# Optimization experiments

Measured on AMD Instinct MI355X. Metric: run time of the kernel, lower is better.

## Reference

```python
import jax, jax.numpy as jnp
import numpy as np

B, K, D = 8, 4000, 256
H, DQ, DV = 8, 32, 32
WIN, PAD = 200, 50
STEP = WIN - 2 * PAD  # 100
BETA = 0.25


def setup_inputs() -> dict:
    key = jax.random.key(0)
    ks = jax.random.split(key, 14)
    s = 0.02
    return {
        "query": jax.random.normal(ks[0], (B, K, D), jnp.float32),
        "key": jax.random.normal(ks[1], (B, K, D), jnp.float32),
        "value": jax.random.normal(ks[2], (B, K, D), jnp.float32),
        "Wq": jax.random.normal(ks[3], (D, H * DQ), jnp.float32) * s,
        "bq": jax.random.normal(ks[4], (H * DQ,), jnp.float32) * s,
        "Wk": jax.random.normal(ks[5], (D, H * DQ), jnp.float32) * s,
        "bk": jax.random.normal(ks[6], (H * DQ,), jnp.float32) * s,
        "Wv": jax.random.normal(ks[7], (D, H * DV), jnp.float32) * s,
        "bv": jax.random.normal(ks[8], (H * DV,), jnp.float32) * s,
        "Wo": jax.random.normal(ks[9], (H * DV, D), jnp.float32) * s,
        "bo": jax.random.normal(ks[10], (D,), jnp.float32) * s,
    }


def _windows(x, n_win):
    starts = jnp.arange(n_win) * STEP
    idx = starts[:, None] + jnp.arange(WIN)[None, :]
    return x[:, :, idx, :]


def reference(query, key, value, Wq, bq, Wk, bk, Wv, bv, Wo, bo):
    b, k_len, d = query.shape
    pad = lambda t: jnp.pad(t, ((0, 0), (PAD, PAD), (0, 0)), mode='edge')  # replicate pad
    qp, kp, vp = pad(query), pad(key), pad(value)
    kpad = k_len + 2 * PAD
    n_win = (kpad - WIN) // STEP + 1

    def proj(x, Wm, bias, dh):
        y = x @ Wm + bias                       # [B, Kp, H*dh]
        return y.reshape(b, kpad, H, dh).transpose(0, 2, 1, 3)  # [B, H, Kp, dh]

    q = _windows(proj(qp, Wq, bq, DQ), n_win)
    kk = _windows(proj(kp, Wk, bk, DQ), n_win)
    v = _windows(proj(vp, Wv, bv, DV), n_win)

    scores = jnp.einsum('bhnid,bhnjd->bhnij', q, kk) / jnp.sqrt(jnp.float32(WIN))
    dist = jnp.abs(jnp.arange(WIN)[:, None] - jnp.arange(WIN)[None, :]).astype(scores.dtype)
    cauchy = (1.0 / (1.0 + BETA * dist * dist)) * (1.0 - jnp.eye(WIN, dtype=scores.dtype))
    scores = scores * cauchy
    causal = jnp.triu(jnp.ones((WIN, WIN), dtype=bool), k=1)  # attention_size is not None -> causal masking
    scores = jnp.where(causal, -jnp.inf, scores)
    attn = jax.nn.softmax(scores, axis=-1)
    out = jnp.einsum('bhnij,bhnjd->bhnid', attn, v)
    out = out[:, :, :, PAD:WIN - PAD, :].reshape(b, H, k_len, DV)
    out = out.transpose(0, 2, 1, 3).reshape(b, k_len, H * DV)  # heads concatenated, head-major slices
    return out @ Wo + bo
```

## Files before the change

kernel.cpp:

```cpp
#include <hip/hip_runtime.h>


typedef __bf16 bf16_t;
typedef __bf16 bf16x8 __attribute__((ext_vector_type(8)));
typedef float  f32x4  __attribute__((ext_vector_type(4)));

#define MFMA16(a, b, c) __builtin_amdgcn_mfma_f32_16x16x32_bf16((a), (b), (c), 0, 0, 0)

static __device__ __forceinline__ bf16x8 cvt8(float4 a, float4 b) {
  bf16x8 r;
  r[0] = (bf16_t)a.x; r[1] = (bf16_t)a.y; r[2] = (bf16_t)a.z; r[3] = (bf16_t)a.w;
  r[4] = (bf16_t)b.x; r[5] = (bf16_t)b.y; r[6] = (bf16_t)b.z; r[7] = (bf16_t)b.w;
  return r;
}

static __device__ __forceinline__ unsigned short bbits(bf16_t v) {
  union { bf16_t b; unsigned short u; } c; c.b = v; return c.u;
}

__global__ __launch_bounds__(256)
void prep_weights(const float* __restrict__ Wq, const float* __restrict__ Wk,
                  const float* __restrict__ Wv, const float* __restrict__ Wo,
                  bf16_t* __restrict__ wt) {
  const int mat  = blockIdx.x >> 6;
  const int tile = blockIdx.x & 63;
  const int kt = (tile >> 3) * 32, nt = (tile & 7) * 32;
  const float* W = (mat == 0) ? Wq : (mat == 1) ? Wk : (mat == 2) ? Wv : Wo;
  __shared__ float t[32][33];
  const int tx = threadIdx.x & 31, ty = threadIdx.x >> 5;
#pragma unroll
  for (int i = 0; i < 32; i += 8)
    t[ty + i][tx] = W[(size_t)(kt + ty + i) * 256 + nt + tx];
  __syncthreads();
  bf16_t* dst = wt + (size_t)mat * 65536;
#pragma unroll
  for (int i = 0; i < 32; i += 8)
    dst[(size_t)(nt + ty + i) * 256 + kt + tx] = (bf16_t)t[tx][ty + i];
}

__global__ __launch_bounds__(256)
void proj_gemm(const float* __restrict__ qx, const float* __restrict__ kx,
               const float* __restrict__ vx, const bf16_t* __restrict__ wt,
               const float* __restrict__ bq, const float* __restrict__ bk,
               const float* __restrict__ bv,
               bf16_t* __restrict__ qb, bf16_t* __restrict__ kb,
               bf16_t* __restrict__ vt, int M, float qscale) {
  const int mode = blockIdx.y;
  const float* X    = (mode == 0) ? qx : (mode == 1) ? kx : vx;
  const float* bias = (mode == 0) ? bq : (mode == 1) ? bk : bv;
  const bf16_t* W   = wt + (size_t)mode * 65536;

  __shared__ bf16_t la[64 * 40];
  __shared__ bf16_t lb[256 * 40];
  const int tid  = threadIdx.x;
  const int lane = tid & 63;
  const int wv   = tid >> 6;
  const int lo   = lane & 15, hi = lane >> 4;
  const int m0   = blockIdx.x * 64;
  int ar = m0 + (tid >> 2); if (ar >= M) ar = M - 1;
  const int acg  = (tid & 3) * 8;
  const int brow = tid >> 2;
  const int bcg  = (tid & 3) * 8;

  f32x4 acc[4][4] = {};

  for (int kk = 0; kk < 256; kk += 32) {
    {
      const float* ap = X + (size_t)ar * 256 + kk + acg;
      *(bf16x8*)&la[(tid >> 2) * 40 + acg] =
          cvt8(((const float4*)ap)[0], ((const float4*)ap)[1]);
    }
#pragma unroll
    for (int rr = 0; rr < 4; ++rr) {
      const int row = brow + rr * 64;
      *(bf16x8*)&lb[row * 40 + bcg] =
          *(const bf16x8*)&W[(size_t)row * 256 + kk + bcg];
    }
    __syncthreads();

    bf16x8 af[4], bfv[4];
#pragma unroll
    for (int mi = 0; mi < 4; ++mi)
      af[mi] = *(const bf16x8*)&la[(mi * 16 + lo) * 40 + hi * 8];
#pragma unroll
    for (int ni = 0; ni < 4; ++ni)
      bfv[ni] = *(const bf16x8*)&lb[(wv * 64 + ni * 16 + lo) * 40 + hi * 8];
#pragma unroll
    for (int mi = 0; mi < 4; ++mi)
#pragma unroll
      for (int ni = 0; ni < 4; ++ni)
        acc[mi][ni] = MFMA16(af[mi], bfv[ni], acc[mi][ni]);
    __syncthreads();
  }

#pragma unroll
  for (int mi = 0; mi < 4; ++mi) {
    const int mb = m0 + mi * 16 + hi * 4;
    if (mb >= M) continue;
#pragma unroll
    for (int ni = 0; ni < 4; ++ni) {
      const int n = wv * 64 + ni * 16 + lo;
      const float bia = bias[n];
      if (mode == 0) {
#pragma unroll
        for (int r = 0; r < 4; ++r)
          qb[(size_t)(mb + r) * 256 + n] = (bf16_t)((acc[mi][ni][r] + bia) * qscale);
      } else if (mode == 1) {
        const int b = mb / 4000, t = mb - b * 4000;
#pragma unroll
        for (int r = 0; r < 4; ++r)
          kb[((size_t)b * 4064 + t + 50 + r) * 256 + n] = (bf16_t)(acc[mi][ni][r] + bia);
      } else {
        const int b = mb / 4000, t = mb - b * 4000;
        const int h = n >> 5, dv = n & 31;
        bf16_t* O = vt + ((size_t)((b * 8 + h) * 32 + dv)) * 4064 + t + 50;
        unsigned short e0 = bbits((bf16_t)(acc[mi][ni][0] + bia));
        unsigned short e1 = bbits((bf16_t)(acc[mi][ni][1] + bia));
        unsigned short e2 = bbits((bf16_t)(acc[mi][ni][2] + bia));
        unsigned short e3 = bbits((bf16_t)(acc[mi][ni][3] + bia));
        unsigned* O32 = (unsigned*)O;
        O32[0] = (unsigned)e0 | ((unsigned)e1 << 16);
        O32[1] = (unsigned)e2 | ((unsigned)e3 << 16);
      }
    }
  }
}

__global__ __launch_bounds__(256)
void out_gemm(const bf16_t* __restrict__ ao, const bf16_t* __restrict__ wt,
              const float* __restrict__ bias, float* __restrict__ Out, int M) {
  __shared__ bf16_t la[64 * 40];
  __shared__ bf16_t lb[256 * 40];
  const int tid  = threadIdx.x;
  const int lane = tid & 63;
  const int wv   = tid >> 6;
  const int lo   = lane & 15, hi = lane >> 4;
  const int m0   = blockIdx.x * 64;
  int ar = m0 + (tid >> 2); if (ar >= M) ar = M - 1;
  const int acg  = (tid & 3) * 8;
  const int brow = tid >> 2;
  const int bcg  = (tid & 3) * 8;

  f32x4 acc[4][4] = {};

  for (int kk = 0; kk < 256; kk += 32) {
    *(bf16x8*)&la[(tid >> 2) * 40 + acg] =
        *(const bf16x8*)&ao[(size_t)ar * 256 + kk + acg];
#pragma unroll
    for (int rr = 0; rr < 4; ++rr) {
      const int row = brow + rr * 64;
      *(bf16x8*)&lb[row * 40 + bcg] =
          *(const bf16x8*)&wt[(size_t)row * 256 + kk + bcg];
    }
    __syncthreads();

    bf16x8 af[4], bfv[4];
#pragma unroll
    for (int mi = 0; mi < 4; ++mi)
      af[mi] = *(const bf16x8*)&la[(mi * 16 + lo) * 40 + hi * 8];
#pragma unroll
    for (int ni = 0; ni < 4; ++ni)
      bfv[ni] = *(const bf16x8*)&lb[(wv * 64 + ni * 16 + lo) * 40 + hi * 8];
#pragma unroll
    for (int mi = 0; mi < 4; ++mi)
#pragma unroll
      for (int ni = 0; ni < 4; ++ni)
        acc[mi][ni] = MFMA16(af[mi], bfv[ni], acc[mi][ni]);
    __syncthreads();
  }

#pragma unroll
  for (int mi = 0; mi < 4; ++mi) {
    const int mb = m0 + mi * 16 + hi * 4;
    if (mb >= M) continue;
#pragma unroll
    for (int ni = 0; ni < 4; ++ni) {
      const int n = wv * 64 + ni * 16 + lo;
      const float bia = bias[n];
#pragma unroll
      for (int r = 0; r < 4; ++r)
        Out[(size_t)(mb + r) * 256 + n] = acc[mi][ni][r] + bia;
    }
  }
}

__global__ void fill_edges(bf16_t* __restrict__ kb, bf16_t* __restrict__ vt, int nb) {
  const int idx = blockIdx.x * 256 + threadIdx.x;
  const int kcnt = nb * 64 * 256;
  if (idx < kcnt) {
    const int b  = idx >> 14;
    const int pp = (idx >> 8) & 63;
    const int nn = idx & 255;
    const int p  = (pp < 50) ? pp : pp + 4000;
    bf16_t v = (pp < 50) ? kb[((size_t)b * 4064 + 50) * 256 + nn] : (bf16_t)0.f;
    kb[((size_t)b * 4064 + p) * 256 + nn] = v;
  } else {
    const int j  = idx - kcnt;
    const int bh = j >> 11;
    const int dv = (j >> 6) & 31;
    const int pp = j & 63;
    const int p  = (pp < 50) ? pp : pp + 4000;
    bf16_t v = (pp < 50) ? vt[((size_t)bh * 32 + dv) * 4064 + 50] : (bf16_t)0.f;
    vt[((size_t)bh * 32 + dv) * 4064 + p] = v;
  }
}

__global__ __launch_bounds__(448)
void attn_win(const bf16_t* __restrict__ qb, const bf16_t* __restrict__ kb,
              const bf16_t* __restrict__ vt, bf16_t* __restrict__ ao) {
  const int blk = blockIdx.x;
  const int n = blk % 40;
  const int h = (blk / 40) & 7;
  const int b = blk / 320;
  const int wv = threadIdx.x >> 6;
  const int lane = threadIdx.x & 63;
  const int lo = lane & 15, hi = lane >> 4;

  __shared__ __align__(16) bf16_t E[7][16][40];

  const int i0 = 50 + 16 * wv;
  int jtmax = (65 + 16 * wv) >> 4;
  if (jtmax > 9) jtmax = 9;
  const int reach = jtmax * 16 + 16;

  int tq = n * 100 + 16 * wv + lo;
  if (tq > 3999) tq = 3999;
  const bf16x8 qf = *(const bf16x8*)&qb[((size_t)b * 4000 + tq) * 256 + h * 32 + hi * 8];

  const f32x4 zero = {0.f, 0.f, 0.f, 0.f};
  bf16x8 onesf;
#pragma unroll
  for (int u = 0; u < 8; ++u) onesf[u] = (bf16_t)1.0f;

  f32x4 o0 = zero, o1 = zero, sm = zero;
  const size_t vbase = ((size_t)((b * 8 + h) * 32)) * 4064 + n * 100;
  const size_t kbase = ((size_t)(b * 4064 + n * 100)) * 256 + h * 32 + hi * 8;
  const int dbase = i0 + hi * 4 - lo;

#pragma unroll
  for (int kt = 0; kt < 5; ++kt) if (kt * 32 < reach) {
#pragma unroll
    for (int half = 0; half < 2; ++half) {
      const int jt = kt * 2 + half;
      if (jt <= jtmax) {
        const bf16x8 kf = *(const bf16x8*)&kb[kbase + (size_t)(jt * 16 + lo) * 256];
        const f32x4 s = MFMA16(qf, kf, zero);
#pragma unroll
        for (int r = 0; r < 4; ++r) {
          const int d = dbase + r - jt * 16;
          const float df = (float)d;
          float c = __builtin_amdgcn_rcpf(__builtin_fmaf(0.25f * df, df, 1.f));
          c = (d == 0) ? 0.f : c;
          float e = __expf(s[r] * c);
          e = (d < 0) ? 0.f : e;
          E[wv][hi * 4 + r][half * 16 + lo] = (bf16_t)e;
        }
      } else {
#pragma unroll
        for (int r = 0; r < 4; ++r)
          E[wv][hi * 4 + r][half * 16 + lo] = (bf16_t)0.f;
      }
    }
    const bf16x8 pf = *(const bf16x8*)&E[wv][lo][hi * 8];
    const bf16x8 v0 = *(const bf16x8*)&vt[vbase + (size_t)lo * 4064 + kt * 32 + hi * 8];
    const bf16x8 v1 = *(const bf16x8*)&vt[vbase + (size_t)(16 + lo) * 4064 + kt * 32 + hi * 8];
    o0 = MFMA16(pf, v0, o0);
    o1 = MFMA16(pf, v1, o1);
    sm = MFMA16(pf, onesf, sm);
  }

#pragma unroll
  for (int r = 0; r < 4; ++r) {
    const int i = i0 + hi * 4 + r;
    if (i < 150) {
      const float ri = __builtin_amdgcn_rcpf(sm[r]);
      const int t = n * 100 + i - 50;
      bf16_t* op = &ao[((size_t)b * 4000 + t) * 256 + h * 32];
      op[lo]      = (bf16_t)(o0[r] * ri);
      op[16 + lo] = (bf16_t)(o1[r] * ri);
    }
  }
}

extern "C" void kernel_launch(void* const* d_in, const int* in_sizes, int n_in,
                              void* d_out, int out_size, void* d_ws, size_t ws_size,
                              hipStream_t stream) {
  (void)in_sizes; (void)n_in; (void)out_size;
  const float* query = (const float*)d_in[0];
  const float* key   = (const float*)d_in[1];
  const float* value = (const float*)d_in[2];
  const float* Wq = (const float*)d_in[3];
  const float* bq = (const float*)d_in[4];
  const float* Wk = (const float*)d_in[5];
  const float* bk = (const float*)d_in[6];
  const float* Wv = (const float*)d_in[7];
  const float* bv = (const float*)d_in[8];
  const float* Wo = (const float*)d_in[9];
  const float* bo = (const float*)d_in[10];

  int bc = 8;
  while (bc > 1 && 524288ull + (unsigned long long)bc * 8257536ull > (unsigned long long)ws_size)
    bc >>= 1;

  bf16_t* wt = (bf16_t*)d_ws;
  bf16_t* qb = wt + 4 * 65536;
  bf16_t* kb = qb + (size_t)bc * 4000 * 256;
  bf16_t* vt = kb + (size_t)bc * 4064 * 256;
  bf16_t* ao = vt + (size_t)bc * 8 * 32 * 4064;

  prep_weights<<<256, 256, 0, stream>>>(Wq, Wk, Wv, Wo, wt);

  const float qscale = 0.07071067811865475f;

  for (int b0 = 0; b0 < 8; b0 += bc) {
    const int M = bc * 4000;
    const int mblk = (M + 63) / 64;
    const float* qx = query + (size_t)b0 * 4000 * 256;
    const float* kx = key   + (size_t)b0 * 4000 * 256;
    const float* vx = value + (size_t)b0 * 4000 * 256;
    float* ox = (float*)d_out + (size_t)b0 * 4000 * 256;

    proj_gemm<<<dim3(mblk, 3), 256, 0, stream>>>(qx, kx, vx, wt, bq, bk, bv,
                                                 qb, kb, vt, M, qscale);
    fill_edges<<<bc * 128, 256, 0, stream>>>(kb, vt, bc);
    attn_win<<<bc * 320, 448, 0, stream>>>(qb, kb, vt, ao);
    out_gemm<<<dim3(mblk), 256, 0, stream>>>(ao, wt + 3 * 65536, bo, ox, M);
  }
}
```

Measured before the change: 97.24 us.

## Hold weight fragments in registers and stage full A tile once in GEMMs

```diff
diff --git a/kernel.cpp b/kernel.cpp
--- a/kernel.cpp
+++ b/kernel.cpp
@@ -38,7 +38,9 @@
     dst[(size_t)(nt + ty + i) * 256 + kt + tx] = (bf16_t)t[tx][ty + i];
 }
 
-__global__ __launch_bounds__(256)
+#define LDSA_BYTES (32 * 1040)
+
+__global__ __launch_bounds__(256, 2)
 void proj_gemm(const float* __restrict__ qx, const float* __restrict__ kx,
                const float* __restrict__ vx, const bf16_t* __restrict__ wt,
                const float* __restrict__ bq, const float* __restrict__ bk,
@@ -50,47 +52,45 @@
   const float* bias = (mode == 0) ? bq : (mode == 1) ? bk : bv;
   const bf16_t* W   = wt + (size_t)mode * 65536;
 
-  __shared__ bf16_t la[64 * 40];
-  __shared__ bf16_t lb[256 * 40];
+  __shared__ __align__(16) char lds_a[LDSA_BYTES];
   const int tid  = threadIdx.x;
   const int lane = tid & 63;
   const int wv   = tid >> 6;
   const int lo   = lane & 15, hi = lane >> 4;
   const int m0   = blockIdx.x * 64;
-  int ar = m0 + (tid >> 2); if (ar >= M) ar = M - 1;
-  const int acg  = (tid & 3) * 8;
-  const int brow = tid >> 2;
-  const int bcg  = (tid & 3) * 8;
+  const int r    = tid >> 2;
+  const int q    = tid & 3;
+  int ar = m0 + r; if (ar >= M) ar = M - 1;
+
+  bf16x8 breg[8][4];
+#pragma unroll
+  for (int kk = 0; kk < 8; ++kk)
+#pragma unroll
+    for (int ni = 0; ni < 4; ++ni)
+      breg[kk][ni] =
+          *(const bf16x8*)&W[(size_t)(wv * 64 + ni * 16 + lo) * 256 + kk * 32 + hi * 8];
+
+#pragma unroll
+  for (int i = 0; i < 8; ++i) {
+    const int c = q * 8 + i;
+    const float* ap = X + (size_t)ar * 256 + c * 8;
+    const bf16x8 v = cvt8(((const float4*)ap)[0], ((const float4*)ap)[1]);
+    *(bf16x8*)(lds_a + c * 1040 + r * 16) = v;
+  }
+  __syncthreads();
 
   f32x4 acc[4][4] = {};
-
-  for (int kk = 0; kk < 256; kk += 32) {
-    {
-      const float* ap = X + (size_t)ar * 256 + kk + acg;
-      *(bf16x8*)&la[(tid >> 2) * 40 + acg] =
-          cvt8(((const float4*)ap)[0], ((const float4*)ap)[1]);
-    }
-#pragma unroll
-    for (int rr = 0; rr < 4; ++rr) {
-      const int row = brow + rr * 64;
-      *(bf16x8*)&lb[row * 40 + bcg] =
-          *(const bf16x8*)&W[(size_t)row * 256 + kk + bcg];
-    }
-    __syncthreads();
-
-    bf16x8 af[4], bfv[4];
+#pragma unroll
+  for (int kk = 0; kk < 8; ++kk) {
+    bf16x8 af[4];
 #pragma unroll
     for (int mi = 0; mi < 4; ++mi)
-      af[mi] = *(const bf16x8*)&la[(mi * 16 + lo) * 40 + hi * 8];
-#pragma unroll
-    for (int ni = 0; ni < 4; ++ni)
-      bfv[ni] = *(const bf16x8*)&lb[(wv * 64 + ni * 16 + lo) * 40 + hi * 8];
+      af[mi] = *(const bf16x8*)(lds_a + (kk * 4 + hi) * 1040 + (mi * 16 + lo) * 16);
 #pragma unroll
     for (int mi = 0; mi < 4; ++mi)
 #pragma unroll
       for (int ni = 0; ni < 4; ++ni)
-        acc[mi][ni] = MFMA16(af[mi], bfv[ni], acc[mi][ni]);
-    __syncthreads();
+        acc[mi][ni] = MFMA16(af[mi], breg[kk][ni], acc[mi][ni]);
   }
 
 #pragma unroll
@@ -103,13 +103,13 @@
       const float bia = bias[n];
       if (mode == 0) {
 #pragma unroll
-        for (int r = 0; r < 4; ++r)
-          qb[(size_t)(mb + r) * 256 + n] = (bf16_t)((acc[mi][ni][r] + bia) * qscale);
+        for (int rr = 0; rr < 4; ++rr)
+          qb[(size_t)(mb + rr) * 256 + n] = (bf16_t)((acc[mi][ni][rr] + bia) * qscale);
       } else if (mode == 1) {
         const int b = mb / 4000, t = mb - b * 4000;
 #pragma unroll
-        for (int r = 0; r < 4; ++r)
-          kb[((size_t)b * 4064 + t + 50 + r) * 256 + n] = (bf16_t)(acc[mi][ni][r] + bia);
+        for (int rr = 0; rr < 4; ++rr)
+          kb[((size_t)b * 4064 + t + 50 + rr) * 256 + n] = (bf16_t)(acc[mi][ni][rr] + bia);
       } else {
         const int b = mb / 4000, t = mb - b * 4000;
         const int h = n >> 5, dv = n & 31;
@@ -126,47 +126,47 @@
   }
 }
 
-__global__ __launch_bounds__(256)
+__global__ __launch_bounds__(256, 2)
 void out_gemm(const bf16_t* __restrict__ ao, const bf16_t* __restrict__ wt,
               const float* __restrict__ bias, float* __restrict__ Out, int M) {
-  __shared__ bf16_t la[64 * 40];
-  __shared__ bf16_t lb[256 * 40];
+  __shared__ __align__(16) char lds_a[LDSA_BYTES];
   const int tid  = threadIdx.x;
   const int lane = tid & 63;
   const int wv   = tid >> 6;
   const int lo   = lane & 15, hi = lane >> 4;
   const int m0   = blockIdx.x * 64;
-  int ar = m0 + (tid >> 2); if (ar >= M) ar = M - 1;
-  const int acg  = (tid & 3) * 8;
-  const int brow = tid >> 2;
-  const int bcg  = (tid & 3) * 8;
+  const int r    = tid >> 2;
+  const int q    = tid & 3;
+  int ar = m0 + r; if (ar >= M) ar = M - 1;
+
+  bf16x8 breg[8][4];
+#pragma unroll
+  for (int kk = 0; kk < 8; ++kk)
+#pragma unroll
+    for (int ni = 0; ni < 4; ++ni)
+      breg[kk][ni] =
+          *(const bf16x8*)&wt[(size_t)(wv * 64 + ni * 16 + lo) * 256 + kk * 32 + hi * 8];
+
+#pragma unroll
+  for (int i = 0; i < 8; ++i) {
+    const int c = q * 8 + i;
+    const bf16x8 v = *(const bf16x8*)&ao[(size_t)ar * 256 + c * 8];
+    *(bf16x8*)(lds_a + c * 1040 + r * 16) = v;
+  }
+  __syncthreads();
 
   f32x4 acc[4][4] = {};
-
-  for (int kk = 0; kk < 256; kk += 32) {
-    *(bf16x8*)&la[(tid >> 2) * 40 + acg] =
-        *(const bf16x8*)&ao[(size_t)ar * 256 + kk + acg];
-#pragma unroll
-    for (int rr = 0; rr < 4; ++rr) {
-      const int row = brow + rr * 64;
-      *(bf16x8*)&lb[row * 40 + bcg] =
-          *(const bf16x8*)&wt[(size_t)row * 256 + kk + bcg];
-    }
-    __syncthreads();
-
-    bf16x8 af[4], bfv[4];
+#pragma unroll
+  for (int kk = 0; kk < 8; ++kk) {
+    bf16x8 af[4];
 #pragma unroll
     for (int mi = 0; mi < 4; ++mi)
-      af[mi] = *(const bf16x8*)&la[(mi * 16 + lo) * 40 + hi * 8];
-#pragma unroll
-    for (int ni = 0; ni < 4; ++ni)
-      bfv[ni] = *(const bf16x8*)&lb[(wv * 64 + ni * 16 + lo) * 40 + hi * 8];
+      af[mi] = *(const bf16x8*)(lds_a + (kk * 4 + hi) * 1040 + (mi * 16 + lo) * 16);
 #pragma unroll
     for (int mi = 0; mi < 4; ++mi)
 #pragma unroll
       for (int ni = 0; ni < 4; ++ni)
-        acc[mi][ni] = MFMA16(af[mi], bfv[ni], acc[mi][ni]);
-    __syncthreads();
+        acc[mi][ni] = MFMA16(af[mi], breg[kk][ni], acc[mi][ni]);
   }
 
 #pragma unroll
@@ -178,8 +178,8 @@
       const int n = wv * 64 + ni * 16 + lo;
       const float bia = bias[n];
 #pragma unroll
-      for (int r = 0; r < 4; ++r)
-        Out[(size_t)(mb + r) * 256 + n] = acc[mi][ni][r] + bia;
+      for (int rr = 0; rr < 4; ++rr)
+        Out[(size_t)(mb + rr) * 256 + n] = acc[mi][ni][rr] + bia;
     }
   }
 }
```

Measured after the change: 119.5 us. +22.9%, slower.

## Retile projection and output GEMMs to 128x128 with direct global-to-LDS loads

Applied to the files above, without the earlier changes.

```diff
diff --git a/kernel.cpp b/kernel.cpp
--- a/kernel.cpp
+++ b/kernel.cpp
@@ -6,6 +6,13 @@
 typedef float  f32x4  __attribute__((ext_vector_type(4)));
 
 #define MFMA16(a, b, c) __builtin_amdgcn_mfma_f32_16x16x32_bf16((a), (b), (c), 0, 0, 0)
+
+typedef __attribute__((address_space(1))) const unsigned char gas_u8;
+typedef __attribute__((address_space(3))) unsigned char las_u8;
+
+static __device__ __forceinline__ void gload16(const void* g, void* l) {
+  __builtin_amdgcn_global_load_lds((gas_u8*)g, (las_u8*)l, 16, 0, 0);
+}
 
 static __device__ __forceinline__ bf16x8 cvt8(float4 a, float4 b) {
   bf16x8 r;
@@ -38,6 +45,7 @@
     dst[(size_t)(nt + ty + i) * 256 + kt + tx] = (bf16_t)t[tx][ty + i];
 }
 
+
 __global__ __launch_bounds__(256)
 void proj_gemm(const float* __restrict__ qx, const float* __restrict__ kx,
                const float* __restrict__ vx, const bf16_t* __restrict__ wt,
@@ -45,46 +53,65 @@
                const float* __restrict__ bv,
                bf16_t* __restrict__ qb, bf16_t* __restrict__ kb,
                bf16_t* __restrict__ vt, int M, float qscale) {
-  const int mode = blockIdx.y;
+  const int mode = blockIdx.z;
   const float* X    = (mode == 0) ? qx : (mode == 1) ? kx : vx;
   const float* bias = (mode == 0) ? bq : (mode == 1) ? bk : bv;
   const bf16_t* W   = wt + (size_t)mode * 65536;
 
-  __shared__ bf16_t la[64 * 40];
-  __shared__ bf16_t lb[256 * 40];
+  __shared__ bf16_t la[128 * 40];
+  __shared__ __align__(16) char ldsB[8192];
   const int tid  = threadIdx.x;
   const int lane = tid & 63;
-  const int wv   = tid >> 6;
+  const int w4   = tid >> 6;
+  const int wr   = ((tid >> 7) & 1) * 64;
+  const int wc   = ((tid >> 6) & 1) * 64;
   const int lo   = lane & 15, hi = lane >> 4;
-  const int m0   = blockIdx.x * 64;
-  int ar = m0 + (tid >> 2); if (ar >= M) ar = M - 1;
-  const int acg  = (tid & 3) * 8;
-  const int brow = tid >> 2;
-  const int bcg  = (tid & 3) * 8;
+  const int m0   = blockIdx.x * 128;
+  const int n0   = blockIdx.y * 128;
+  const int arow = tid >> 1;
+  const int acol = (tid & 1) * 16;
+  int ar = m0 + arow; if (ar >= M) ar = M - 1;
+
+  const bf16_t* bsrc[2];
+  char* bldst[2];
+#pragma unroll
+  for (int j = 0; j < 2; ++j) {
+    const int s = (w4 * 2 + j) * 64 + lane;
+    const int row = s >> 2, cs = s & 3;
+    const int c = cs ^ ((row >> 2) & 3);
+    bsrc[j]  = W + (size_t)(n0 + row) * 256 + c * 8;
+    bldst[j] = ldsB + (w4 * 2 + j) * 1024;
+  }
+  int bbase[4];
+#pragma unroll
+  for (int ni = 0; ni < 4; ++ni) {
+    const int row = wc + ni * 16 + lo;
+    bbase[ni] = (row * 4 + (hi ^ ((lo >> 2) & 3))) * 16;
+  }
 
   f32x4 acc[4][4] = {};
 
   for (int kk = 0; kk < 256; kk += 32) {
     {
-      const float* ap = X + (size_t)ar * 256 + kk + acg;
-      *(bf16x8*)&la[(tid >> 2) * 40 + acg] =
-          cvt8(((const float4*)ap)[0], ((const float4*)ap)[1]);
-    }
-#pragma unroll
-    for (int rr = 0; rr < 4; ++rr) {
-      const int row = brow + rr * 64;
-      *(bf16x8*)&lb[row * 40 + bcg] =
-          *(const bf16x8*)&W[(size_t)row * 256 + kk + bcg];
-    }
+      const float* ap = X + (size_t)ar * 256 + kk + acol;
+      float4 x0 = ((const float4*)ap)[0];
+      float4 x1 = ((const float4*)ap)[1];
+      float4 x2 = ((const float4*)ap)[2];
+      float4 x3 = ((const float4*)ap)[3];
+      *(bf16x8*)&la[arow * 40 + acol]     = cvt8(x0, x1);
+      *(bf16x8*)&la[arow * 40 + acol + 8] = cvt8(x2, x3);
+    }
+    gload16(bsrc[0] + kk, bldst[0]);
+    gload16(bsrc[1] + kk, bldst[1]);
     __syncthreads();
 
     bf16x8 af[4], bfv[4];
 #pragma unroll
     for (int mi = 0; mi < 4; ++mi)
-      af[mi] = *(const bf16x8*)&la[(mi * 16 + lo) * 40 + hi * 8];
+      af[mi] = *(const bf16x8*)&la[(wr + mi * 16 + lo) * 40 + hi * 8];
 #pragma unroll
     for (int ni = 0; ni < 4; ++ni)
-      bfv[ni] = *(const bf16x8*)&lb[(wv * 64 + ni * 16 + lo) * 40 + hi * 8];
+      bfv[ni] = *(const bf16x8*)(ldsB + bbase[ni]);
 #pragma unroll
     for (int mi = 0; mi < 4; ++mi)
 #pragma unroll
@@ -95,21 +122,21 @@
 
 #pragma unroll
   for (int mi = 0; mi < 4; ++mi) {
-    const int mb = m0 + mi * 16 + hi * 4;
+    const int mb = m0 + wr + mi * 16 + hi * 4;
     if (mb >= M) continue;
 #pragma unroll
     for (int ni = 0; ni < 4; ++ni) {
-      const int n = wv * 64 + ni * 16 + lo;
+      const int n = n0 + wc + ni * 16 + lo;
       const float bia = bias[n];
       if (mode == 0) {
 #pragma unroll
-        for (int r = 0; r < 4; ++r)
-          qb[(size_t)(mb + r) * 256 + n] = (bf16_t)((acc[mi][ni][r] + bia) * qscale);
+        for (int rr = 0; rr < 4; ++rr)
+          qb[(size_t)(mb + rr) * 256 + n] = (bf16_t)((acc[mi][ni][rr] + bia) * qscale);
       } else if (mode == 1) {
         const int b = mb / 4000, t = mb - b * 4000;
 #pragma unroll
-        for (int r = 0; r < 4; ++r)
-          kb[((size_t)b * 4064 + t + 50 + r) * 256 + n] = (bf16_t)(acc[mi][ni][r] + bia);
+        for (int rr = 0; rr < 4; ++rr)
+          kb[((size_t)b * 4064 + t + 50 + rr) * 256 + n] = (bf16_t)(acc[mi][ni][rr] + bia);
       } else {
         const int b = mb / 4000, t = mb - b * 4000;
         const int h = n >> 5, dv = n & 31;
@@ -129,38 +156,56 @@
 __global__ __launch_bounds__(256)
 void out_gemm(const bf16_t* __restrict__ ao, const bf16_t* __restrict__ wt,
               const float* __restrict__ bias, float* __restrict__ Out, int M) {
-  __shared__ bf16_t la[64 * 40];
-  __shared__ bf16_t lb[256 * 40];
+  __shared__ __align__(16) char ldsA[8192];
+  __shared__ __align__(16) char ldsB[8192];
   const int tid  = threadIdx.x;
   const int lane = tid & 63;
-  const int wv   = tid >> 6;
+  const int w4   = tid >> 6;
+  const int wr   = ((tid >> 7) & 1) * 64;
+  const int wc   = ((tid >> 6) & 1) * 64;
   const int lo   = lane & 15, hi = lane >> 4;
-  const int m0   = blockIdx.x * 64;
-  int ar = m0 + (tid >> 2); if (ar >= M) ar = M - 1;
-  const int acg  = (tid & 3) * 8;
-  const int brow = tid >> 2;
-  const int bcg  = (tid & 3) * 8;
+  const int m0   = blockIdx.x * 128;
+  const int n0   = blockIdx.y * 128;
+
+  const bf16_t* asrc[2];
+  const bf16_t* bsrc[2];
+  char *aldst[2], *bldst[2];
+#pragma unroll
+  for (int j = 0; j < 2; ++j) {
+    const int s = (w4 * 2 + j) * 64 + lane;
+    const int row = s >> 2, cs = s & 3;
+    const int c = cs ^ ((row >> 2) & 3);
+    int arw = m0 + row; if (arw >= M) arw = M - 1;
+    asrc[j]  = ao + (size_t)arw * 256 + c * 8;
+    aldst[j] = ldsA + (w4 * 2 + j) * 1024;
+    bsrc[j]  = wt + (size_t)(n0 + row) * 256 + c * 8;
+    bldst[j] = ldsB + (w4 * 2 + j) * 1024;
+  }
+  int abase[4], bbase[4];
+#pragma unroll
+  for (int i = 0; i < 4; ++i) {
+    const int arw = wr + i * 16 + lo;
+    abase[i] = (arw * 4 + (hi ^ ((lo >> 2) & 3))) * 16;
+    const int brw = wc + i * 16 + lo;
+    bbase[i] = (brw * 4 + (hi ^ ((lo >> 2) & 3))) * 16;
+  }
 
   f32x4 acc[4][4] = {};
 
   for (int kk = 0; kk < 256; kk += 32) {
-    *(bf16x8*)&la[(tid >> 2) * 40 + acg] =
-        *(const bf16x8*)&ao[(size_t)ar * 256 + kk + acg];
-#pragma unroll
-    for (int rr = 0; rr < 4; ++rr) {
-      const int row = brow + rr * 64;
-      *(bf16x8*)&lb[row * 40 + bcg] =
-          *(const bf16x8*)&wt[(size_t)row * 256 + kk + bcg];
-    }
+    gload16(asrc[0] + kk, aldst[0]);
+    gload16(asrc[1] + kk, aldst[1]);
+    gload16(bsrc[0] + kk, bldst[0]);
+    gload16(bsrc[1] + kk, bldst[1]);
     __syncthreads();
 
     bf16x8 af[4], bfv[4];
 #pragma unroll
     for (int mi = 0; mi < 4; ++mi)
-      af[mi] = *(const bf16x8*)&la[(mi * 16 + lo) * 40 + hi * 8];
+      af[mi] = *(const bf16x8*)(ldsA + abase[mi]);
 #pragma unroll
     for (int ni = 0; ni < 4; ++ni)
-      bfv[ni] = *(const bf16x8*)&lb[(wv * 64 + ni * 16 + lo) * 40 + hi * 8];
+      bfv[ni] = *(const bf16x8*)(ldsB + bbase[ni]);
 #pragma unroll
     for (int mi = 0; mi < 4; ++mi)
 #pragma unroll
@@ -171,15 +216,15 @@
 
 #pragma unroll
   for (int mi = 0; mi < 4; ++mi) {
-    const int mb = m0 + mi * 16 + hi * 4;
+    const int mb = m0 + wr + mi * 16 + hi * 4;
     if (mb >= M) continue;
 #pragma unroll
     for (int ni = 0; ni < 4; ++ni) {
-      const int n = wv * 64 + ni * 16 + lo;
+      const int n = n0 + wc + ni * 16 + lo;
       const float bia = bias[n];
 #pragma unroll
-      for (int r = 0; r < 4; ++r)
-        Out[(size_t)(mb + r) * 256 + n] = acc[mi][ni][r] + bia;
+      for (int rr = 0; rr < 4; ++rr)
+        Out[(size_t)(mb + rr) * 256 + n] = acc[mi][ni][rr] + bia;
     }
   }
 }
@@ -314,16 +359,16 @@
 
   for (int b0 = 0; b0 < 8; b0 += bc) {
     const int M = bc * 4000;
-    const int mblk = (M + 63) / 64;
+    const int mblk = (M + 127) / 128;
     const float* qx = query + (size_t)b0 * 4000 * 256;
     const float* kx = key   + (size_t)b0 * 4000 * 256;
     const float* vx = value + (size_t)b0 * 4000 * 256;
     float* ox = (float*)d_out + (size_t)b0 * 4000 * 256;
 
-    proj_gemm<<<dim3(mblk, 3), 256, 0, stream>>>(qx, kx, vx, wt, bq, bk, bv,
-                                                 qb, kb, vt, M, qscale);
+    proj_gemm<<<dim3(mblk, 2, 3), 256, 0, stream>>>(qx, kx, vx, wt, bq, bk, bv,
+                                                    qb, kb, vt, M, qscale);
     fill_edges<<<bc * 128, 256, 0, stream>>>(kb, vt, bc);
     attn_win<<<bc * 320, 448, 0, stream>>>(qb, kb, vt, ao);
-    out_gemm<<<dim3(mblk), 256, 0, stream>>>(ao, wt + 3 * 65536, bo, ox, M);
-  }
-}
+    out_gemm<<<dim3(mblk, 2), 256, 0, stream>>>(ao, wt + 3 * 65536, bo, ox, M);
+  }
+}
```

Result: slower. 104.7 us (+7.7%).
